# Performance work log

Measured on AMD Instinct MI355X. Metric: run time of the kernel, lower is better.

Reference implementation:

```python
import jax, jax.numpy as jnp
import numpy as np

K = 1024          # num_embeddings
D = 128           # embedding_dim
BETA = 0.25
DECAY = 0.99
EPS = 1e-05
RESTART_THRESHOLD = 0.5


def setup_inputs() -> dict:
    key = jax.random.key(0)
    k1, k2, k3 = jax.random.split(key, 3)
    B, L = 8, 4096
    z_e = jax.random.normal(k1, (B, D, L), dtype=jnp.float32)
    # nn.init.uniform_(embedding, -1/K, 1/K)
    embedding = jax.random.uniform(k2, (K, D), dtype=jnp.float32,
                                   minval=-1.0 / K, maxval=1.0 / K)
    cluster_size = jnp.zeros((K,), dtype=jnp.float32)
    embedding_avg = embedding.copy()
    return {"z_e": z_e, "embedding": embedding,
            "cluster_size": cluster_size, "embedding_avg": embedding_avg}


def reference(z_e, embedding, cluster_size, embedding_avg):
    """Training-mode forward of EMAVectorQuantizer (1D latents, z_e: (B, D, L)).

    Note: in the torch code `e = self.embedding` aliases the buffer, and
    self.embedding.data.copy_(embed_normalized) mutates it in-place BEFORE
    z_q_flat = encodings @ e, so quantization uses the UPDATED codebook.
    We reproduce that ordering here. Random-restart indices use a fixed key.
    """
    B, Dd, L = z_e.shape
    # (B, D, L) -> (B, L, D) -> (N, D)
    z_flat = jnp.transpose(z_e, (0, 2, 1)).reshape(-1, Dd)  # N = B*L
    N = z_flat.shape[0]

    # squared-euclidean distances (N, K) via expansion
    z_sq = jnp.sum(z_flat * z_flat, axis=1, keepdims=True)          # (N, 1)
    e_sq = jnp.sum(embedding * embedding, axis=1)                   # (K,)
    distances = z_sq + e_sq[None, :] - 2.0 * (z_flat @ embedding.T)  # (N, K)
    indices = jnp.argmin(distances, axis=1)                          # (N,)

    # EMA updates (one-hot sums expressed as segment sums)
    counts = jax.ops.segment_sum(jnp.ones((N,), z_flat.dtype), indices, num_segments=K)
    new_cluster = DECAY * cluster_size + (1.0 - DECAY) * counts      # (K,)
    weighted_sum = jax.ops.segment_sum(z_flat, indices, num_segments=K)  # (K, D)
    new_avg = DECAY * embedding_avg + (1.0 - DECAY) * weighted_sum

    # random restart of dead codes (fixed key for determinism)
    dead = new_cluster < RESTART_THRESHOLD                           # (K,) bool
    ridx = jax.random.randint(jax.random.key(42), (K,), 0, N)
    rvec = z_flat[ridx]                                              # (K, D)
    new_cluster = jnp.where(dead, RESTART_THRESHOLD, new_cluster)
    new_avg = jnp.where(dead[:, None], rvec * RESTART_THRESHOLD, new_avg)

    # Laplace-smoothed normalization -> updated codebook
    n = jnp.sum(new_cluster)
    smoothed = (new_cluster + EPS) / (n + K * EPS) * n
    new_embedding = new_avg / smoothed[:, None]                      # (K, D)

    # quantize with the UPDATED codebook (matches torch aliasing semantics)
    z_q_flat = new_embedding[indices]                                # (N, D)
    z_q = jnp.transpose(z_q_flat.reshape(B, L, Dd), (0, 2, 1))       # (B, D, L)

    sg = jax.lax.stop_gradient
    codebook_loss = jnp.mean((sg(z_e) - z_q) ** 2)
    commitment_loss = jnp.mean((z_e - sg(z_q)) ** 2)
    vq_loss = codebook_loss + BETA * commitment_loss

    z_q_st = z_e + sg(z_q - z_e)
    indices_map = indices.reshape(B, L)
    return (z_q_st, indices_map, vq_loss, codebook_loss, BETA * commitment_loss)
```

## Files before the change

### kernel.cpp

```cpp
#include <hip/hip_runtime.h>
#include <stdint.h>

constexpr int BB = 8;
constexpr int LL = 4096;
constexpr int DD = 128;
constexpr int KC = 1024;
constexpr int NN = BB * LL;
constexpr int ZTOT = BB * DD * LL;

#define THREEFRY_PARTITIONABLE 1

typedef float f32x16 __attribute__((ext_vector_type(16)));
typedef short s16x8 __attribute__((ext_vector_type(8)));

union F4S8 { float4 f; s16x8 s; };

__device__ __forceinline__ ushort f2bf(float x) {
  uint32_t u = __float_as_uint(x);
  uint32_t r = u + 0x7FFFu + ((u >> 16) & 1u);
  return (ushort)(r >> 16);
}
__device__ __forceinline__ float bf2f(ushort h) {
  return __uint_as_float(((uint32_t)h) << 16);
}

__device__ __forceinline__ uint32_t rotl32(uint32_t x, int r) {
  return (x << r) | (x >> (32 - r));
}

__device__ __forceinline__ void threefry2x32(uint32_t k0, uint32_t k1,
                                             uint32_t x0, uint32_t x1,
                                             uint32_t* o0, uint32_t* o1) {
  uint32_t ks0 = k0, ks1 = k1, ks2 = 0x1BD11BDAu ^ k0 ^ k1;
  x0 += ks0; x1 += ks1;
  x0 += x1; x1 = rotl32(x1, 13); x1 ^= x0;
  x0 += x1; x1 = rotl32(x1, 15); x1 ^= x0;
  x0 += x1; x1 = rotl32(x1, 26); x1 ^= x0;
  x0 += x1; x1 = rotl32(x1, 6);  x1 ^= x0;
  x0 += ks1; x1 += ks2 + 1u;
  x0 += x1; x1 = rotl32(x1, 17); x1 ^= x0;
  x0 += x1; x1 = rotl32(x1, 29); x1 ^= x0;
  x0 += x1; x1 = rotl32(x1, 16); x1 ^= x0;
  x0 += x1; x1 = rotl32(x1, 24); x1 ^= x0;
  x0 += ks2; x1 += ks0 + 2u;
  x0 += x1; x1 = rotl32(x1, 13); x1 ^= x0;
  x0 += x1; x1 = rotl32(x1, 15); x1 ^= x0;
  x0 += x1; x1 = rotl32(x1, 26); x1 ^= x0;
  x0 += x1; x1 = rotl32(x1, 6);  x1 ^= x0;
  x0 += ks0; x1 += ks1 + 3u;
  x0 += x1; x1 = rotl32(x1, 17); x1 ^= x0;
  x0 += x1; x1 = rotl32(x1, 29); x1 ^= x0;
  x0 += x1; x1 = rotl32(x1, 16); x1 ^= x0;
  x0 += x1; x1 = rotl32(x1, 24); x1 ^= x0;
  x0 += ks1; x1 += ks2 + 4u;
  x0 += x1; x1 = rotl32(x1, 13); x1 ^= x0;
  x0 += x1; x1 = rotl32(x1, 15); x1 ^= x0;
  x0 += x1; x1 = rotl32(x1, 26); x1 ^= x0;
  x0 += x1; x1 = rotl32(x1, 6);  x1 ^= x0;
  x0 += ks2; x1 += ks0 + 5u;
  *o0 = x0; *o1 = x1;
}

__global__ __launch_bounds__(128) void k_prep(const float* __restrict__ E,
                                              float* __restrict__ esq,
                                              double* __restrict__ lacc,
                                              ushort* __restrict__ E0f,
                                              ushort* __restrict__ E1f) {
  const int k = blockIdx.x;
  const int d = threadIdx.x;
  float v = E[k * DD + d];
  __shared__ float r[128];
  __shared__ ushort sh0[128], sh1[128];
  ushort h0 = f2bf(v);
  float v0 = bf2f(h0);
  ushort h1 = f2bf(v - v0);
  sh0[d] = h0; sh1[d] = h1;
  r[d] = v * v;
  __syncthreads();
  for (int s = 64; s > 0; s >>= 1) {
    if (d < s) r[d] += r[d + s];
    __syncthreads();
  }
  if (d == 0) {
    esq[k] = r[0];
    if (k == 0) lacc[0] = 0.0;
  }
  if (d < 32) {
    const ushort* src = (d < 16) ? sh0 : sh1;
    ushort* dst = (d < 16) ? E0f : E1f;
    int p = d & 15, h = p & 1, ks = p >> 1;
    int slot = ((k >> 5) * 8 + ks) * 64 + (k & 31) + 32 * h;
    int off = ks * 16 + h * 8;
    uint32_t w0 = (uint32_t)src[off + 0] | ((uint32_t)src[off + 1] << 16);
    uint32_t w1 = (uint32_t)src[off + 2] | ((uint32_t)src[off + 3] << 16);
    uint32_t w2 = (uint32_t)src[off + 4] | ((uint32_t)src[off + 5] << 16);
    uint32_t w3 = (uint32_t)src[off + 6] | ((uint32_t)src[off + 7] << 16);
    uint4 val; val.x = w0; val.y = w1; val.z = w2; val.w = w3;
    *(uint4*)(dst + (size_t)slot * 8) = val;
  }
}

__global__ __launch_bounds__(256, 4) void k_dist(const float* __restrict__ Z,
                                                 const float* __restrict__ E,
                                                 const ushort* __restrict__ E0f,
                                                 const ushort* __restrict__ E1f,
                                                 const float* __restrict__ esq,
                                                 int* __restrict__ idx_out,
                                                 float* __restrict__ zflat) {
  __shared__ float Zt[128][33];
  __shared__ float esh[1024];
  __shared__ float mv1[4][32], mv2[4][32];
  __shared__ int   mi1[4][32], mi2[4][32];

  const int tid = threadIdx.x;
  const int w = tid >> 6;
  const int lane = tid & 63;
  const int hi = lane >> 5;
  const int rr = lane & 31;
  const int r0 = blockIdx.x * 32;
  const int b = r0 >> 12;
  const int l0 = r0 & (LL - 1);

  const float* zsrc = Z + (size_t)b * DD * LL + l0;
#pragma unroll
  for (int p = 0; p < 4; ++p) {
    int f = p * 256 + tid;
    int d = f >> 3;
    int g = f & 7;
    float4 v = *(const float4*)(zsrc + (size_t)d * LL + g * 4);
    Zt[d][g * 4 + 0] = v.x;
    Zt[d][g * 4 + 1] = v.y;
    Zt[d][g * 4 + 2] = v.z;
    Zt[d][g * 4 + 3] = v.w;
  }
  {
    float4 e4 = *(const float4*)(esq + tid * 4);
    *(float4*)(&esh[tid * 4]) = e4;
  }
  __syncthreads();

  {
    float* dst = zflat + (size_t)r0 * DD;
#pragma unroll
    for (int p = 0; p < 4; ++p) {
      int f = p * 256 + tid;
      int row = f >> 5;
      int dq = f & 31;
      float4 v;
      v.x = Zt[dq * 4 + 0][row];
      v.y = Zt[dq * 4 + 1][row];
      v.z = Zt[dq * 4 + 2][row];
      v.w = Zt[dq * 4 + 3][row];
      *(float4*)(dst + (size_t)row * DD + dq * 4) = v;
    }
  }

  s16x8 B0[8], B1[8];
#pragma unroll
  for (int ks = 0; ks < 8; ++ks) {
    s16x8 b0, b1;
#pragma unroll
    for (int j = 0; j < 8; ++j) {
      float z = Zt[ks * 16 + hi * 8 + j][rr];
      ushort h0 = f2bf(z);
      float z0f = bf2f(h0);
      ushort h1 = f2bf(z - z0f);
      b0[j] = (short)h0;
      b1[j] = (short)h1;
    }
    B0[ks] = b0; B1[ks] = b1;
  }

  float b1v = 3.4e38f, b2v = 3.4e38f;
  int b1i = 0, b2i = 0;
  const float4* e0p = (const float4*)E0f;
  const float4* e1p = (const float4*)E1f;

  for (int s = 0; s < 8; ++s) {
    const int sg = w * 8 + s;
    f32x16 acc;
#pragma unroll
    for (int i = 0; i < 16; ++i) acc[i] = 0.0f;
    const int base = sg * 512 + lane;
#pragma unroll
    for (int ks = 0; ks < 8; ++ks) {
      F4S8 ua, ub;
      ua.f = e0p[base + ks * 64];
      ub.f = e1p[base + ks * 64];
      acc = __builtin_amdgcn_mfma_f32_32x32x16_bf16(ua.s, B0[ks], acc, 0, 0, 0);
      acc = __builtin_amdgcn_mfma_f32_32x32x16_bf16(ua.s, B1[ks], acc, 0, 0, 0);
      acc = __builtin_amdgcn_mfma_f32_32x32x16_bf16(ub.s, B0[ks], acc, 0, 0, 0);
    }
#pragma unroll
    for (int reg = 0; reg < 16; ++reg) {
      int cl = (reg & 3) + 8 * (reg >> 2) + 4 * hi;
      int c = sg * 32 + cl;
      float rv = fmaf(-2.0f, acc[reg], esh[c]);
      if (rv < b1v) { b2v = b1v; b2i = b1i; b1v = rv; b1i = c; }
      else if (rv < b2v) { b2v = rv; b2i = c; }
    }
  }

  float ov1 = __shfl_xor(b1v, 32, 64); int oi1 = __shfl_xor(b1i, 32, 64);
  float ov2 = __shfl_xor(b2v, 32, 64); int oi2 = __shfl_xor(b2i, 32, 64);
  if (ov1 < b1v || (ov1 == b1v && oi1 < b1i)) { b2v = b1v; b2i = b1i; b1v = ov1; b1i = oi1; }
  else if (ov1 < b2v || (ov1 == b2v && oi1 < b2i)) { b2v = ov1; b2i = oi1; }
  if (ov2 < b2v || (ov2 == b2v && oi2 < b2i)) { b2v = ov2; b2i = oi2; }

  if (hi == 0) {
    mv1[w][rr] = b1v; mi1[w][rr] = b1i;
    mv2[w][rr] = b2v; mi2[w][rr] = b2i;
  }
  __syncthreads();

  if (tid < 32) {
    const int row = tid;
    float fb1 = mv1[0][row]; int fi1 = mi1[0][row];
    float fb2 = mv2[0][row]; int fi2 = mi2[0][row];
#pragma unroll
    for (int q = 1; q < 4; ++q) {
      float v1 = mv1[q][row]; int i1 = mi1[q][row];
      float v2 = mv2[q][row]; int i2 = mi2[q][row];
      if (v1 < fb1 || (v1 == fb1 && i1 < fi1)) {
        fb2 = fb1; fi2 = fi1; fb1 = v1; fi1 = i1;
      } else if (v1 < fb2 || (v1 == fb2 && i1 < fi2)) {
        fb2 = v1; fi2 = i1;
      }
      if (v2 < fb2 || (v2 == fb2 && i2 < fi2)) { fb2 = v2; fi2 = i2; }
    }

    int fi = fi1;
    if (fb2 - fb1 <= 4e-5f) {
      float zsq = 0.0f;
#pragma unroll 4
      for (int d = 0; d < 128; ++d) {
        float z = Zt[d][row];
        zsq = fmaf(z, z, zsq);
      }
      float dot1 = 0.0f, dot2 = 0.0f;
      const float* e1r = E + (size_t)fi1 * DD;
      const float* e2r = E + (size_t)fi2 * DD;
      for (int d = 0; d < 128; ++d) {
        float z = Zt[d][row];
        dot1 = fmaf(z, e1r[d], dot1);
        dot2 = fmaf(z, e2r[d], dot2);
      }
      float k1 = (zsq + esh[fi1]) - 2.0f * dot1;
      float k2 = (zsq + esh[fi2]) - 2.0f * dot2;
      if (k2 < k1 || (k2 == k1 && fi2 < fi1)) fi = fi2;
    }
    idx_out[r0 + row] = fi;
  }
}

__global__ __launch_bounds__(1024) void k_hist(const int* __restrict__ idxs,
                                               int* __restrict__ part_cnt) {
  __shared__ int h[1024];
  const int tid = threadIdx.x;
  const int j = blockIdx.x;
  h[tid] = 0;
  __syncthreads();
  int k = idxs[j * 1024 + tid];
  atomicAdd(&h[k], 1);
  __syncthreads();
  part_cnt[j * 1024 + tid] = h[tid];
}

__global__ __launch_bounds__(1024) void k_scan(int* __restrict__ part_cnt,
                                               int* __restrict__ code_start,
                                               int* __restrict__ icnt,
                                               float* __restrict__ counts,
                                               const float* __restrict__ cs_in,
                                               float* __restrict__ smooth,
                                               int* __restrict__ ridx,
                                               int* __restrict__ deadf) {
  const int k = threadIdx.x;
  int base[32];
  int s = 0;
#pragma unroll
  for (int j = 0; j < 32; ++j) {
    base[j] = s;
    s += part_cnt[j * 1024 + k];
  }
  icnt[k] = s;
  counts[k] = (float)s;

  __shared__ int ps[1024];
  ps[k] = s;
  __syncthreads();
  for (int off = 1; off < 1024; off <<= 1) {
    int v = (k >= off) ? ps[k - off] : 0;
    __syncthreads();
    ps[k] += v;
    __syncthreads();
  }
  int excl = ps[k] - s;
  code_start[k] = excl;
#pragma unroll
  for (int j = 0; j < 32; ++j) {
    part_cnt[j * 1024 + k] = excl + base[j];
  }

  float c = (float)s;
  float t1 = 0.99f * cs_in[k];
  float t2 = 0.01f * c;
  float nc = t1 + t2;
  bool dead = nc < 0.5f;

  uint32_t bits;
#if THREEFRY_PARTITIONABLE
  {
    uint32_t o0, o1;
    threefry2x32(0u, 42u, 0u, (uint32_t)k, &o0, &o1);
    bits = o0 ^ o1;
  }
#else
  {
    uint32_t o0, o1;
    if (k < 512) { threefry2x32(0u, 42u, (uint32_t)k, (uint32_t)(k + 512), &o0, &o1); bits = o0; }
    else         { threefry2x32(0u, 42u, (uint32_t)(k - 512), (uint32_t)k, &o0, &o1); bits = o1; }
  }
#endif
  int r = (int)(bits & 0x7FFFu);

  float rep = dead ? 0.5f : nc;

  __shared__ float fred[1024];
  fred[k] = rep;
  __syncthreads();
  for (int st = 512; st > 0; st >>= 1) {
    if (k < st) fred[k] += fred[k + st];
    __syncthreads();
  }
  float n = fred[0];

  float sm = ((rep + 1e-5f) / (n + 0.01024f)) * n;
  smooth[k] = sm;
  ridx[k] = r;
  deadf[k] = dead ? 1 : 0;
}

__global__ __launch_bounds__(1024) void k_scatter(const int* __restrict__ idxs,
                                                  const int* __restrict__ part_base,
                                                  int* __restrict__ rowlist) {
  __shared__ int cur[1024];
  const int tid = threadIdx.x;
  const int j = blockIdx.x;
  cur[tid] = part_base[j * 1024 + tid];
  __syncthreads();
  int row = j * 1024 + tid;
  int k = idxs[row];
  int pos = atomicAdd(&cur[k], 1);
  rowlist[pos] = row;
}

__global__ __launch_bounds__(256) void k_wsum2(const float* __restrict__ zflat,
                                               const int* __restrict__ rowlist,
                                               const int* __restrict__ code_start,
                                               const int* __restrict__ icnt,
                                               const float* __restrict__ avg_in,
                                               const float* __restrict__ smooth,
                                               const int* __restrict__ ridx,
                                               const int* __restrict__ deadf,
                                               float* __restrict__ nemb) {
  const int k = blockIdx.x;
  const int tid = threadIdx.x;
  const int h = tid >> 7;
  const int d = tid & 127;
  __shared__ float red[128];

  const int start = code_start[k];
  const int m = icnt[k];
  float acc = 0.0f;
  for (int j = h; j < m; j += 2) {
    int row = rowlist[start + j];
    acc += zflat[(size_t)row * DD + d];
  }
  if (h == 1) red[d] = acc;
  __syncthreads();
  if (h == 0) {
    float wsumv = acc + red[d];
    float t1 = 0.99f * avg_in[k * DD + d];
    float t2 = 0.01f * wsumv;
    float na = t1 + t2;
    if (deadf[k]) {
      int r = ridx[k];
      na = zflat[(size_t)r * DD + d] * 0.5f;
    }
    nemb[k * DD + d] = na / smooth[k];
  }
}

__global__ __launch_bounds__(256) void k_out(const float* __restrict__ Z,
                                             const float* __restrict__ nemb,
                                             const int* __restrict__ idxs,
                                             float* __restrict__ out,
                                             double* __restrict__ lacc) {
  __shared__ float Zt[128][33];
  __shared__ float Ot[128][33];
  __shared__ int sidx[32];
  __shared__ float lred[4];

  const int tid = threadIdx.x;
  const int r0 = blockIdx.x * 32;
  const int b = r0 >> 12;
  const int l0 = r0 & (LL - 1);

  const float* zsrc = Z + (size_t)b * DD * LL + l0;
#pragma unroll
  for (int p = 0; p < 4; ++p) {
    int f = p * 256 + tid;
    int d = f >> 3;
    int g = f & 7;
    float4 v = *(const float4*)(zsrc + (size_t)d * LL + g * 4);
    Zt[d][g * 4 + 0] = v.x;
    Zt[d][g * 4 + 1] = v.y;
    Zt[d][g * 4 + 2] = v.z;
    Zt[d][g * 4 + 3] = v.w;
  }
  if (tid < 32) sidx[tid] = idxs[r0 + tid];
  __syncthreads();

  const int grp = tid >> 5;
  const int ln = tid & 31;
  float lsum = 0.0f;
#pragma unroll
  for (int it = 0; it < 4; ++it) {
    int row = it * 8 + grp;
    int fi = sidx[row];
    float4 q4 = *(const float4*)(nemb + (size_t)fi * DD + ln * 4);
    float z0 = Zt[ln * 4 + 0][row];
    float z1 = Zt[ln * 4 + 1][row];
    float z2 = Zt[ln * 4 + 2][row];
    float z3 = Zt[ln * 4 + 3][row];
    float o0 = z0 + (q4.x - z0);
    float o1 = z1 + (q4.y - z1);
    float o2 = z2 + (q4.z - z2);
    float o3 = z3 + (q4.w - z3);
    Ot[ln * 4 + 0][row] = o0;
    Ot[ln * 4 + 1][row] = o1;
    Ot[ln * 4 + 2][row] = o2;
    Ot[ln * 4 + 3][row] = o3;
    float d0 = z0 - q4.x, d1 = z1 - q4.y, d2 = z2 - q4.z, d3 = z3 - q4.w;
    lsum += d0 * d0 + d1 * d1 + d2 * d2 + d3 * d3;
  }
  __syncthreads();

  float* dstz = out + (size_t)b * DD * LL + l0;
#pragma unroll
  for (int p = 0; p < 4; ++p) {
    int f = p * 256 + tid;
    int d = f >> 3;
    int g = f & 7;
    float4 v;
    v.x = Ot[d][g * 4 + 0];
    v.y = Ot[d][g * 4 + 1];
    v.z = Ot[d][g * 4 + 2];
    v.w = Ot[d][g * 4 + 3];
    *(float4*)(dstz + (size_t)d * LL + g * 4) = v;
  }
  if (tid < 32) out[(size_t)ZTOT + r0 + tid] = (float)sidx[tid];

  for (int off = 32; off > 0; off >>= 1) lsum += __shfl_down(lsum, off, 64);
  if ((tid & 63) == 0) lred[tid >> 6] = lsum;
  __syncthreads();
  if (tid == 0) {
    float tot = (lred[0] + lred[1]) + (lred[2] + lred[3]);
    atomicAdd(lacc, (double)tot);
  }
}

__global__ void k_fin(const double* __restrict__ lacc, float* __restrict__ out) {
  double S = lacc[0];
  float cb = (float)(S / (double)ZTOT);
  float bc = 0.25f * cb;
  float vq = cb + bc;
  float* o = out + (size_t)ZTOT + NN;
  o[0] = vq;
  o[1] = cb;
  o[2] = bc;
}

extern "C" void kernel_launch(void* const* d_in, const int* in_sizes, int n_in,
                              void* d_out, int out_size, void* d_ws, size_t ws_size,
                              hipStream_t stream) {
  const float* Z  = (const float*)d_in[0];
  const float* E  = (const float*)d_in[1];
  const float* CS = (const float*)d_in[2];
  const float* EA = (const float*)d_in[3];
  float* out = (float*)d_out;
  float* ws = (float*)d_ws;

  float* counts = ws;
  float* esq    = ws + 1024;
  float* smooth = ws + 2048;
  int*   ridx   = (int*)(ws + 3072);
  int*   deadf  = (int*)(ws + 4096);
  float* nemb   = ws + 8192 + 131072;
  int*   idxs   = (int*)(ws + 270336);
  double* lacc  = (double*)(ws + 303104);

  int* rowlist    = (int*)(ws + 303360);
  int* code_start = (int*)(ws + 336128);
  int* icnt       = (int*)(ws + 337152);

  ushort* E0f = (ushort*)nemb;
  ushort* E1f = (ushort*)(nemb + 65536);
  int* part_cnt = (int*)nemb;

  float* zflat = out;

  k_prep<<<KC, DD, 0, stream>>>(E, esq, lacc, E0f, E1f);
  k_dist<<<NN / 32, 256, 0, stream>>>(Z, E, E0f, E1f, esq, idxs, zflat);
  k_hist<<<32, 1024, 0, stream>>>(idxs, part_cnt);
  k_scan<<<1, 1024, 0, stream>>>(part_cnt, code_start, icnt, counts,
                                 CS, smooth, ridx, deadf);
  k_scatter<<<32, 1024, 0, stream>>>(idxs, part_cnt, rowlist);
  k_wsum2<<<KC, 256, 0, stream>>>(zflat, rowlist, code_start, icnt,
                                  EA, smooth, ridx, deadf, nemb);
  k_out<<<NN / 32, 256, 0, stream>>>(Z, nemb, idxs, out, lacc);
  k_fin<<<1, 1, 0, stream>>>(lacc, out);
}
```

Measured before the change: 104.6 us.

## Fuse histogram into distance kernel and split MFMA accumulator chains

Removes the separate k_hist kernel. Code counts are now built with global atomics at the end of k_dist, k_scan reads the single histogram, and k_scatter uses global atomic cursors instead of per-block shared cursors. The MFMA inner loop also uses two independent accumulators so dependent MFMA chains can overlap. The risks are contention on global atomics for popular codes, nondeterministic row ordering within a code's list, and a slightly different summation order in the distance dot product.

```diff
diff --git a/kernel.cpp b/kernel.cpp
--- a/kernel.cpp
+++ b/kernel.cpp
@@ -65,7 +65,8 @@
                                               float* __restrict__ esq,
                                               double* __restrict__ lacc,
                                               ushort* __restrict__ E0f,
-                                              ushort* __restrict__ E1f) {
+                                              ushort* __restrict__ E1f,
+                                              int* __restrict__ ihist) {
   const int k = blockIdx.x;
   const int d = threadIdx.x;
   float v = E[k * DD + d];
@@ -83,6 +84,7 @@
   }
   if (d == 0) {
     esq[k] = r[0];
+    ihist[k] = 0;
     if (k == 0) lacc[0] = 0.0;
   }
   if (d < 32) {
@@ -106,7 +108,8 @@
                                                  const ushort* __restrict__ E1f,
                                                  const float* __restrict__ esq,
                                                  int* __restrict__ idx_out,
-                                                 float* __restrict__ zflat) {
+                                                 float* __restrict__ zflat,
+                                                 int* __restrict__ ihist) {
   __shared__ float Zt[128][33];
   __shared__ float esh[1024];
   __shared__ float mv1[4][32], mv2[4][32];
@@ -178,24 +181,30 @@
 
   for (int s = 0; s < 8; ++s) {
     const int sg = w * 8 + s;
-    f32x16 acc;
-#pragma unroll
-    for (int i = 0; i < 16; ++i) acc[i] = 0.0f;
+    f32x16 accA, accB;
+#pragma unroll
+    for (int i = 0; i < 16; ++i) { accA[i] = 0.0f; accB[i] = 0.0f; }
     const int base = sg * 512 + lane;
 #pragma unroll
-    for (int ks = 0; ks < 8; ++ks) {
-      F4S8 ua, ub;
+    for (int ks = 0; ks < 4; ++ks) {
+      F4S8 ua, ub, uc, ud;
       ua.f = e0p[base + ks * 64];
       ub.f = e1p[base + ks * 64];
-      acc = __builtin_amdgcn_mfma_f32_32x32x16_bf16(ua.s, B0[ks], acc, 0, 0, 0);
-      acc = __builtin_amdgcn_mfma_f32_32x32x16_bf16(ua.s, B1[ks], acc, 0, 0, 0);
-      acc = __builtin_amdgcn_mfma_f32_32x32x16_bf16(ub.s, B0[ks], acc, 0, 0, 0);
+      uc.f = e0p[base + (ks + 4) * 64];
+      ud.f = e1p[base + (ks + 4) * 64];
+      accA = __builtin_amdgcn_mfma_f32_32x32x16_bf16(ua.s, B0[ks], accA, 0, 0, 0);
+      accB = __builtin_amdgcn_mfma_f32_32x32x16_bf16(uc.s, B0[ks + 4], accB, 0, 0, 0);
+      accA = __builtin_amdgcn_mfma_f32_32x32x16_bf16(ua.s, B1[ks], accA, 0, 0, 0);
+      accB = __builtin_amdgcn_mfma_f32_32x32x16_bf16(uc.s, B1[ks + 4], accB, 0, 0, 0);
+      accA = __builtin_amdgcn_mfma_f32_32x32x16_bf16(ub.s, B0[ks], accA, 0, 0, 0);
+      accB = __builtin_amdgcn_mfma_f32_32x32x16_bf16(ud.s, B0[ks + 4], accB, 0, 0, 0);
     }
 #pragma unroll
     for (int reg = 0; reg < 16; ++reg) {
       int cl = (reg & 3) + 8 * (reg >> 2) + 4 * hi;
       int c = sg * 32 + cl;
-      float rv = fmaf(-2.0f, acc[reg], esh[c]);
+      float dot = accA[reg] + accB[reg];
+      float rv = fmaf(-2.0f, dot, esh[c]);
       if (rv < b1v) { b2v = b1v; b2i = b1i; b1v = rv; b1i = c; }
       else if (rv < b2v) { b2v = rv; b2i = c; }
     }
@@ -250,38 +259,21 @@
       if (k2 < k1 || (k2 == k1 && fi2 < fi1)) fi = fi2;
     }
     idx_out[r0 + row] = fi;
-  }
-}
-
-__global__ __launch_bounds__(1024) void k_hist(const int* __restrict__ idxs,
-                                               int* __restrict__ part_cnt) {
-  __shared__ int h[1024];
-  const int tid = threadIdx.x;
-  const int j = blockIdx.x;
-  h[tid] = 0;
-  __syncthreads();
-  int k = idxs[j * 1024 + tid];
-  atomicAdd(&h[k], 1);
-  __syncthreads();
-  part_cnt[j * 1024 + tid] = h[tid];
-}
-
-__global__ __launch_bounds__(1024) void k_scan(int* __restrict__ part_cnt,
+    atomicAdd(&ihist[fi], 1);
+  }
+}
+
+__global__ __launch_bounds__(1024) void k_scan(const int* __restrict__ ihist,
                                                int* __restrict__ code_start,
                                                int* __restrict__ icnt,
+                                               int* __restrict__ cur_g,
                                                float* __restrict__ counts,
                                                const float* __restrict__ cs_in,
                                                float* __restrict__ smooth,
                                                int* __restrict__ ridx,
                                                int* __restrict__ deadf) {
   const int k = threadIdx.x;
-  int base[32];
-  int s = 0;
-#pragma unroll
-  for (int j = 0; j < 32; ++j) {
-    base[j] = s;
-    s += part_cnt[j * 1024 + k];
-  }
+  int s = ihist[k];
   icnt[k] = s;
   counts[k] = (float)s;
 
@@ -296,10 +288,7 @@
   }
   int excl = ps[k] - s;
   code_start[k] = excl;
-#pragma unroll
-  for (int j = 0; j < 32; ++j) {
-    part_cnt[j * 1024 + k] = excl + base[j];
-  }
+  cur_g[k] = excl;
 
   float c = (float)s;
   float t1 = 0.99f * cs_in[k];
@@ -341,16 +330,13 @@
 }
 
 __global__ __launch_bounds__(1024) void k_scatter(const int* __restrict__ idxs,
-                                                  const int* __restrict__ part_base,
+                                                  int* __restrict__ cur_g,
                                                   int* __restrict__ rowlist) {
-  __shared__ int cur[1024];
   const int tid = threadIdx.x;
   const int j = blockIdx.x;
-  cur[tid] = part_base[j * 1024 + tid];
-  __syncthreads();
   int row = j * 1024 + tid;
   int k = idxs[row];
-  int pos = atomicAdd(&cur[k], 1);
+  int pos = atomicAdd(&cur_g[k], 1);
   rowlist[pos] = row;
 }
 
@@ -503,19 +489,19 @@
   int* rowlist    = (int*)(ws + 303360);
   int* code_start = (int*)(ws + 336128);
   int* icnt       = (int*)(ws + 337152);
+  int* ihist      = (int*)(ws + 338176);
+  int* cur_g      = (int*)(ws + 339200);
 
   ushort* E0f = (ushort*)nemb;
   ushort* E1f = (ushort*)(nemb + 65536);
-  int* part_cnt = (int*)nemb;
 
   float* zflat = out;
 
-  k_prep<<<KC, DD, 0, stream>>>(E, esq, lacc, E0f, E1f);
-  k_dist<<<NN / 32, 256, 0, stream>>>(Z, E, E0f, E1f, esq, idxs, zflat);
-  k_hist<<<32, 1024, 0, stream>>>(idxs, part_cnt);
-  k_scan<<<1, 1024, 0, stream>>>(part_cnt, code_start, icnt, counts,
+  k_prep<<<KC, DD, 0, stream>>>(E, esq, lacc, E0f, E1f, ihist);
+  k_dist<<<NN / 32, 256, 0, stream>>>(Z, E, E0f, E1f, esq, idxs, zflat, ihist);
+  k_scan<<<1, 1024, 0, stream>>>(ihist, code_start, icnt, cur_g, counts,
                                  CS, smooth, ridx, deadf);
-  k_scatter<<<32, 1024, 0, stream>>>(idxs, part_cnt, rowlist);
+  k_scatter<<<32, 1024, 0, stream>>>(idxs, cur_g, rowlist);
   k_wsum2<<<KC, 256, 0, stream>>>(zflat, rowlist, code_start, icnt,
                                   EA, smooth, ridx, deadf, nemb);
   k_out<<<NN / 32, 256, 0, stream>>>(Z, nemb, idxs, out, lacc);
```

Result: slower. 108.6 us (+3.8%).
